# Optimization experiments

Hardware: AMD Instinct MI355X
Metric: run time of the kernel (lower is better)

Reference implementation:

```python
import jax, jax.numpy as jnp
import numpy as np

NUM_HEAD = 16


def setup_inputs() -> dict:
    key = jax.random.key(0)
    ks = jax.random.split(key, 4)
    B, C, D = 2, 2048, 1024
    hidden_states = jax.random.normal(ks[0], (B, C, D), dtype=jnp.float32)
    attention_mask = jnp.zeros((B, 1, C, C), dtype=jnp.float32)
    Wqkv = jax.random.normal(ks[1], (D, 3 * D), dtype=jnp.float32) * (D ** -0.5)
    bqkv = jnp.zeros((3 * D,), dtype=jnp.float32)
    Wo = jax.random.normal(ks[2], (D, D), dtype=jnp.float32) * (D ** -0.5)
    bo = jnp.zeros((D,), dtype=jnp.float32)
    return {"hidden_states": hidden_states, "attention_mask": attention_mask,
            "Wqkv": Wqkv, "bqkv": bqkv, "Wo": Wo, "bo": bo}


def reference(hidden_states, attention_mask, Wqkv, bqkv, Wo, bo):
    B, C, D = hidden_states.shape
    H = NUM_HEAD
    hd = D // H
    scaling = hd ** -0.5

    qkv = hidden_states @ Wqkv + bqkv                      # [B, C, 3D]
    q, k, v = jnp.split(qkv, 3, axis=-1)
    # [B, C, H, hd] -> [B, H, C, hd]
    q = q.reshape(B, C, H, hd).transpose(0, 2, 1, 3)
    k = k.reshape(B, C, H, hd).transpose(0, 2, 1, 3)
    v = v.reshape(B, C, H, hd).transpose(0, 2, 1, 3)

    scores = jnp.einsum("bhqd,bhkd->bhqk", q, k) * scaling  # [B, H, C, C]
    causal = jnp.tril(jnp.ones((C, C), dtype=bool))[None, None]
    mask = jnp.where(causal, attention_mask, -jnp.inf)      # [B, 1, C, C]
    probs = jax.nn.softmax(scores + mask, axis=-1)
    out = jnp.einsum("bhqk,bhkd->bhqd", probs, v)           # [B, H, C, hd]
    out = out.transpose(0, 2, 1, 3).reshape(B, C, D)
    return out @ Wo + bo
```

## Files before the change

### kernel.cpp

```cpp
#include <hip/hip_runtime.h>
#include <hip/hip_bf16.h>
#include <cstdint>
#include <cstddef>

typedef __attribute__((ext_vector_type(8))) short short8;
typedef __attribute__((ext_vector_type(4))) float f32x4;
typedef __attribute__((ext_vector_type(16))) float f32x16;
typedef __attribute__((ext_vector_type(4))) unsigned int u32x4;
typedef unsigned short u16;
typedef unsigned int u32;

#define B_ 2
#define C_ 2048
#define D_ 1024
#define H_ 16
#define HD_ 64
#define LOG2E 1.4426950408889634f

static __device__ __forceinline__ u16 f2b(float f) {
  u32 x = __builtin_bit_cast(u32, f);
  x += 0x7FFFu + ((x >> 16) & 1u);
  return (u16)(x >> 16);
}
static __device__ __forceinline__ float b2f(u16 v) {
  return __builtin_bit_cast(float, (u32)v << 16);
}

__device__ const unsigned char SEGTAB[20] = {
  1, 66, 67, 83, 132, 148, 133, 149, 165, 198, 214, 230, 199, 215, 231, 247,
  0, 82, 164, 246};

__global__ void k_convert(const float* __restrict__ in, u16* __restrict__ out, int n) {
  int i = (blockIdx.x * blockDim.x + threadIdx.x) * 4;
  const int stride = gridDim.x * blockDim.x * 4;
  for (; i < n; i += stride) {
    float4 v = *reinterpret_cast<const float4*>(in + i);
    ushort4 o;
    o.x = f2b(v.x); o.y = f2b(v.y); o.z = f2b(v.z); o.w = f2b(v.w);
    *reinterpret_cast<ushort4*>(out + i) = o;
  }
}

__global__ void k_tconv(const float* __restrict__ in, u16* __restrict__ out, int R, int Cc) {
  __shared__ float tile[64][65];
  const int tC = blockIdx.x * 64;
  const int tR = blockIdx.y * 64;
  const int t = threadIdx.x;
  const int r0 = t >> 4;
  const int c0 = (t & 15) * 4;
#pragma unroll
  for (int ii = 0; ii < 4; ++ii) {
    int r = ii * 16 + r0;
    float4 v = *reinterpret_cast<const float4*>(&in[(size_t)(tR + r) * Cc + tC + c0]);
    tile[r][c0] = v.x; tile[r][c0 + 1] = v.y; tile[r][c0 + 2] = v.z; tile[r][c0 + 3] = v.w;
  }
  __syncthreads();
#pragma unroll
  for (int ii = 0; ii < 4; ++ii) {
    int c = ii * 16 + r0;
    ushort4 o;
    o.x = f2b(tile[c0 + 0][c]);
    o.y = f2b(tile[c0 + 1][c]);
    o.z = f2b(tile[c0 + 2][c]);
    o.w = f2b(tile[c0 + 3][c]);
    *reinterpret_cast<ushort4*>(&out[(size_t)(tC + c) * R + tR + c0]) = o;
  }
}

__global__ void k_maskflags(const float* __restrict__ mask, u32* __restrict__ flags) {
  const int bid = blockIdx.x;
  const int kt = bid & 31, qs = (bid >> 5) & 31, b = bid >> 10;
  const int t = threadIdx.x;
  const float* base = mask + ((size_t)b * C_ + qs * 64) * C_ + kt * 64;
  const int row = t >> 2, c0 = (t & 3) * 16;
  int any = 0;
#pragma unroll
  for (int i = 0; i < 4; ++i) {
    float4 v = *reinterpret_cast<const float4*>(base + (size_t)row * C_ + c0 + i * 4);
    any |= (v.x != 0.f) | (v.y != 0.f) | (v.z != 0.f) | (v.w != 0.f);
  }
  __shared__ int sh[4];
  const unsigned long long bal = __ballot(any);
  if ((t & 63) == 0) sh[t >> 6] = (bal != 0ull);
  __syncthreads();
  if (t == 0) flags[bid] = (u32)(sh[0] | sh[1] | sh[2] | sh[3]);
}

#define GLL16(gptr, lptr) __builtin_amdgcn_global_load_lds( \
    (const __attribute__((address_space(1))) u32*)(gptr),   \
    (__attribute__((address_space(3))) u32*)(lptr), 16, 0, 0)

template<int EPI, int BM>
__global__ __launch_bounds__(256) void k_gemm(
    const u16* __restrict__ A, const u16* __restrict__ Bt,
    int M, int N, int K, const float* __restrict__ bias,
    u16* __restrict__ Cq, u16* __restrict__ Ck, u16* __restrict__ Cv,
    float* __restrict__ Cf)
{
  constexpr int WCW = (BM == 128) ? 64 : 32;
  constexpr int NF = WCW / 16;
  __shared__ __align__(16) u16 As[BM * 64];
  __shared__ __align__(16) u16 Bs[128 * 64];
  const int t = threadIdx.x;
  const int l = t & 63, w = t >> 6;
  const int wr = (BM == 128) ? (w >> 1) : 0;
  const int wc = (BM == 128) ? (w & 1) : w;
  const int lr = l & 15, lg = l >> 4;
  const int swk = lr & 7;
  const int m0 = blockIdx.y * BM, n0 = blockIdx.x * 128;
  f32x4 acc[4][NF] = {};

  for (int k0 = 0; k0 < K; k0 += 64) {
#pragma unroll
    for (int s = 0; s < BM / 32; ++s) {
      const int u = s * 256 + t;
      const int row = u >> 3, slot = (u & 7) ^ (row & 7);
      GLL16(A + (size_t)(m0 + row) * K + k0 + (slot << 3), As + (u << 3));
    }
#pragma unroll
    for (int s = 0; s < 4; ++s) {
      const int u = s * 256 + t;
      const int row = u >> 3, slot = (u & 7) ^ (row & 7);
      GLL16(Bt + (size_t)(n0 + row) * K + k0 + (slot << 3), Bs + (u << 3));
    }
    __syncthreads();
    short8 af[2][4], bfr[2][NF];
#pragma unroll
    for (int s = 0; s < 2; ++s) {
#pragma unroll
      for (int m = 0; m < 4; ++m)
        af[s][m] = *reinterpret_cast<const short8*>(
            &As[((wr * 64 + m * 16 + lr) << 6) + (((s * 4 + lg) ^ swk) << 3)]);
#pragma unroll
      for (int n = 0; n < NF; ++n)
        bfr[s][n] = *reinterpret_cast<const short8*>(
            &Bs[((wc * WCW + n * 16 + lr) << 6) + (((s * 4 + lg) ^ swk) << 3)]);
    }
#pragma unroll
    for (int s = 0; s < 2; ++s)
#pragma unroll
      for (int m = 0; m < 4; ++m)
#pragma unroll
        for (int n = 0; n < NF; ++n)
          acc[m][n] = __builtin_amdgcn_mfma_f32_16x16x32_bf16(af[s][m], bfr[s][n], acc[m][n], 0, 0, 0);
    __syncthreads();
  }

#pragma unroll
  for (int m = 0; m < 4; ++m) {
    const int mg = m0 + wr * 64 + m * 16 + lg * 4;
    const int bq = mg >> 11, c0 = mg & 2047;
#pragma unroll
    for (int n = 0; n < NF; ++n) {
      const int ng = n0 + wc * WCW + n * 16 + lr;
      const float bia = bias[ng];
      if (EPI == 0) {
        const int reg = ng >> 10, d = ng & 1023, h = d >> 6, e = d & 63;
        if (reg == 2) {
          u16* vp = Cv + (((size_t)(bq * H_ + h) * HD_ + e) << 11) + c0;
#pragma unroll
          for (int j = 0; j < 4; ++j) vp[j] = f2b(acc[m][n][j] + bia);
        } else {
          u16* dst = (reg == 0) ? Cq : Ck;
#pragma unroll
          for (int j = 0; j < 4; ++j)
            dst[(((size_t)(bq * H_ + h) * C_ + c0 + j) << 6) + e] = f2b(acc[m][n][j] + bia);
        }
      } else {
#pragma unroll
        for (int j = 0; j < 4; ++j)
          Cf[(size_t)(mg + j) * N + ng] = acc[m][n][j] + bia;
      }
    }
  }
}

static __device__ __forceinline__ void stage_kv(
    const u16* __restrict__ Kbh, const u16* __restrict__ Vbh,
    u16* Kd, u16* Vd, int kt, int t)
{
  const int row = t >> 3, slot = (t & 7) ^ (row & 7);
  GLL16(Kbh + (((size_t)(kt * 64 + row)) << 6) + (slot << 3), Kd + (t << 3));
  GLL16(Vbh + (((size_t)row) << 11) + kt * 64 + (slot << 3), Vd + (t << 3));
}

__global__ __launch_bounds__(512) void k_attn(
    const u16* __restrict__ Q, const u16* __restrict__ Kb, const u16* __restrict__ Vt,
    const float* __restrict__ mask, const u32* __restrict__ flags,
    u16* __restrict__ O, u16* __restrict__ Opart, float2* __restrict__ ml)
{
  __shared__ __align__(16) u16 buf[3 * 8192];
  const int bid = blockIdx.x;
  const int bh = bid & 31;
  const int e = SEGTAB[bid >> 5];
  const int qt = e & 15, seg = (e >> 4) & 3, nseg = (e >> 6) + 1;
  const int ntiles = 4 * qt + 4;
  const int kt0 = seg * 8;
  const int kt1 = (kt0 + 8 < ntiles) ? kt0 + 8 : ntiles;
  const int slotbase = (qt < 4) ? (qt - 2) * 2
                     : (qt < 6) ? 4 + (qt - 4) * 3
                     : 10 + (qt - 6) * 4;
  const int slot = bh * 18 + slotbase + seg;

  const int b = bh >> 4, h = bh & 15;
  const int t = threadIdx.x;
  const int l = t & 63, w = t >> 6;
  const int q = l & 31, hi = l >> 5;
  const int q7 = q & 7;

  const u16* Kbh = Kb + (size_t)bh * (C_ * HD_);
  const u16* Vbh = Vt + (size_t)bh * (HD_ * C_);

  const int q0w = qt * 256 + w * 32;
  const int qg = q0w + q;
  const int qmaxw = q0w + 31;

  short8 aq[4];
  {
    const u16* qp = Q + ((size_t)bh * C_ + qg) * HD_ + hi * 8;
#pragma unroll
    for (int kh = 0; kh < 4; ++kh) {
      short8 v = *reinterpret_cast<const short8*>(qp + kh * 16);
#pragma unroll
      for (int i = 0; i < 8; ++i) {
        const float f = b2f((u16)v[i]) * (0.125f * LOG2E);
        v[i] = (short)f2b(f);
      }
      aq[kh] = v;
    }
  }

  u32 fbits = 0;
  {
    const u32* fp = flags + (size_t)(b * 32 + (q0w >> 6)) * 32 + kt0;
#pragma unroll
    for (int i = 0; i < 8; ++i) fbits |= (fp[i] ? 1u : 0u) << i;
  }

  f32x16 oa0 = {}, oa1 = {};
  float mrun = -INFINITY, srun = 0.f;
  const float* mrow = mask + ((size_t)b * C_ + qg) * C_;

  stage_kv(Kbh, Vbh, buf, buf + 4096, kt0, t);
  if (kt0 + 1 < kt1) stage_kv(Kbh, Vbh, buf + 8192, buf + 8192 + 4096, kt0 + 1, t);

#pragma unroll 1
  for (int kt = kt0; kt < kt1; ++kt) {
    const int bi = (kt - kt0) % 3;
    if (kt + 1 < kt1) asm volatile("s_waitcnt vmcnt(2)" ::: "memory");
    else              asm volatile("s_waitcnt vmcnt(0)" ::: "memory");
    __builtin_amdgcn_s_barrier();
    __builtin_amdgcn_sched_barrier(0);
    if (kt + 2 < kt1) {
      const int bn = (kt + 2 - kt0) % 3;
      stage_kv(Kbh, Vbh, buf + bn * 8192, buf + bn * 8192 + 4096, kt + 2, t);
    }
    if (kt * 64 > qmaxw) continue;

    const char* Kc = reinterpret_cast<const char*>(buf + bi * 8192);
    const char* Vc = reinterpret_cast<const char*>(buf + bi * 8192 + 4096);

    f32x16 p0 = {}, p1 = {};
#pragma unroll
    for (int kh = 0; kh < 4; ++kh) {
      const int sl = ((2 * kh + hi) ^ q7) << 4;
      const short8 k0 = *reinterpret_cast<const short8*>(Kc + q * 128 + sl);
      const short8 k1 = *reinterpret_cast<const short8*>(Kc + (32 + q) * 128 + sl);
      p0 = __builtin_amdgcn_mfma_f32_32x32x16_bf16(k0, aq[kh], p0, 0, 0, 0);
      p1 = __builtin_amdgcn_mfma_f32_32x32x16_bf16(k1, aq[kh], p1, 0, 0, 0);
    }

    if ((fbits >> (kt - kt0)) & 1u) {
      const float* mp = mrow + kt * 64 + 4 * hi;
#pragma unroll
      for (int g = 0; g < 4; ++g) {
        const float4 m0 = *reinterpret_cast<const float4*>(mp + 8 * g);
        const float4 m1 = *reinterpret_cast<const float4*>(mp + 32 + 8 * g);
        p0[4*g+0] = fmaf(m0.x, LOG2E, p0[4*g+0]);
        p0[4*g+1] = fmaf(m0.y, LOG2E, p0[4*g+1]);
        p0[4*g+2] = fmaf(m0.z, LOG2E, p0[4*g+2]);
        p0[4*g+3] = fmaf(m0.w, LOG2E, p0[4*g+3]);
        p1[4*g+0] = fmaf(m1.x, LOG2E, p1[4*g+0]);
        p1[4*g+1] = fmaf(m1.y, LOG2E, p1[4*g+1]);
        p1[4*g+2] = fmaf(m1.z, LOG2E, p1[4*g+2]);
        p1[4*g+3] = fmaf(m1.w, LOG2E, p1[4*g+3]);
      }
    }
    if (kt * 64 + 63 > q0w) {
#pragma unroll
      for (int r = 0; r < 16; ++r) {
        const int kl = kt * 64 + (r & 3) + 8 * (r >> 2) + 4 * hi;
        if (kl > qg) p0[r] = -INFINITY;
        if (kl + 32 > qg) p1[r] = -INFINITY;
      }
    }

    float pm = -INFINITY;
#pragma unroll
    for (int r = 0; r < 16; ++r) pm = fmaxf(pm, fmaxf(p0[r], p1[r]));
    pm = fmaxf(pm, __shfl_xor(pm, 32));
    if (__ballot(pm > mrun) != 0ull) {
      const float mn = fmaxf(fmaxf(mrun, pm), -1e30f);
      const float rs = exp2f(mrun - mn);
      srun *= rs;
      oa0 *= rs; oa1 *= rs;
      mrun = mn;
    }
    float sum = 0.f;
#pragma unroll
    for (int r = 0; r < 16; ++r) {
      p0[r] = exp2f(p0[r] - mrun); sum += p0[r];
      p1[r] = exp2f(p1[r] - mrun); sum += p1[r];
    }
    sum += __shfl_xor(sum, 32);
    srun += sum;

    __builtin_amdgcn_s_setprio(1);
#pragma unroll
    for (int ks = 0; ks < 4; ++ks) {
      const int o = (ks & 1) * 8;
      u32 X, X2, Y, Y2;
      if (ks < 2) {
        asm("v_cvt_pk_bf16_f32 %0, %1, %2" : "=v"(X)  : "v"(p0[o+0]), "v"(p0[o+1]));
        asm("v_cvt_pk_bf16_f32 %0, %1, %2" : "=v"(X2) : "v"(p0[o+2]), "v"(p0[o+3]));
        asm("v_cvt_pk_bf16_f32 %0, %1, %2" : "=v"(Y)  : "v"(p0[o+4]), "v"(p0[o+5]));
        asm("v_cvt_pk_bf16_f32 %0, %1, %2" : "=v"(Y2) : "v"(p0[o+6]), "v"(p0[o+7]));
      } else {
        asm("v_cvt_pk_bf16_f32 %0, %1, %2" : "=v"(X)  : "v"(p1[o+0]), "v"(p1[o+1]));
        asm("v_cvt_pk_bf16_f32 %0, %1, %2" : "=v"(X2) : "v"(p1[o+2]), "v"(p1[o+3]));
        asm("v_cvt_pk_bf16_f32 %0, %1, %2" : "=v"(Y)  : "v"(p1[o+4]), "v"(p1[o+5]));
        asm("v_cvt_pk_bf16_f32 %0, %1, %2" : "=v"(Y2) : "v"(p1[o+6]), "v"(p1[o+7]));
      }
      asm("v_permlane32_swap_b32 %0, %1" : "+v"(X), "+v"(Y));
      asm("v_permlane32_swap_b32 %0, %1" : "+v"(X2), "+v"(Y2));
      const u32x4 bw = {X, X2, Y, Y2};
      const short8 bp = __builtin_bit_cast(short8, bw);
      const int sl = ((2 * ks + hi) ^ q7) << 4;
      const short8 v0 = *reinterpret_cast<const short8*>(Vc + q * 128 + sl);
      const short8 v1 = *reinterpret_cast<const short8*>(Vc + (32 + q) * 128 + sl);
      oa0 = __builtin_amdgcn_mfma_f32_32x32x16_bf16(v0, bp, oa0, 0, 0, 0);
      oa1 = __builtin_amdgcn_mfma_f32_32x32x16_bf16(v1, bp, oa1, 0, 0, 0);
    }
    __builtin_amdgcn_s_setprio(0);
  }

  const float rinv = 1.f / srun;
  const int q2 = l >> 1, hf = l & 1;
#pragma unroll 1
  for (int ph = 0; ph < 2; ++ph) {
    __syncthreads();
    if ((w >> 2) == ph) {
      char* Swb = reinterpret_cast<char*>(buf) + (w & 3) * 4608;
#pragma unroll
      for (int g = 0; g < 4; ++g) {
        const int d0 = 8 * g + 4 * hi;
        const float a0 = oa0[4*g+0] * rinv, a1 = oa0[4*g+1] * rinv;
        const float a2 = oa0[4*g+2] * rinv, a3 = oa0[4*g+3] * rinv;
        const float b0 = oa1[4*g+0] * rinv, b1 = oa1[4*g+1] * rinv;
        const float b2 = oa1[4*g+2] * rinv, b3 = oa1[4*g+3] * rinv;
        u32 w0, w1, w2, w3;
        asm("v_cvt_pk_bf16_f32 %0, %1, %2" : "=v"(w0) : "v"(a0), "v"(a1));
        asm("v_cvt_pk_bf16_f32 %0, %1, %2" : "=v"(w1) : "v"(a2), "v"(a3));
        asm("v_cvt_pk_bf16_f32 %0, %1, %2" : "=v"(w2) : "v"(b0), "v"(b1));
        asm("v_cvt_pk_bf16_f32 %0, %1, %2" : "=v"(w3) : "v"(b2), "v"(b3));
        *reinterpret_cast<uint2*>(Swb + q * 144 + d0 * 2) = make_uint2(w0, w1);
        *reinterpret_cast<uint2*>(Swb + q * 144 + (d0 + 32) * 2) = make_uint2(w2, w3);
      }
      asm volatile("" ::: "memory");
      if (nseg == 1) {
        u16* orow = O + ((size_t)b * C_ + q0w + q2) * D_ + h * 64 + hf * 32;
#pragma unroll
        for (int i = 0; i < 4; ++i) {
          const short8 v = *reinterpret_cast<const short8*>(Swb + q2 * 144 + hf * 64 + i * 16);
          *reinterpret_cast<short8*>(orow + i * 8) = v;
        }
      } else {
        u16* prow = Opart + (((size_t)slot * 256 + w * 32 + q2) << 6) + hf * 32;
#pragma unroll
        for (int i = 0; i < 4; ++i) {
          const short8 v = *reinterpret_cast<const short8*>(Swb + q2 * 144 + hf * 64 + i * 16);
          *reinterpret_cast<short8*>(prow + i * 8) = v;
        }
      }
    }
  }
  if (nseg > 1 && hi == 0)
    ml[(size_t)slot * 256 + w * 32 + q] = make_float2(mrun, srun);
}

__global__ __launch_bounds__(512) void k_merge(
    const u16* __restrict__ Opart, const float2* __restrict__ ml, u16* __restrict__ O)
{
  const int bid = blockIdx.x;
  const int bh = bid & 31;
  const int qt = 2 + (bid >> 5);
  const int nseg = (qt < 4) ? 2 : (qt < 6) ? 3 : 4;
  const int slotbase = (qt < 4) ? (qt - 2) * 2
                     : (qt < 6) ? 4 + (qt - 4) * 3
                     : 10 + (qt - 6) * 4;
  const int slot0 = bh * 18 + slotbase;
  const int b = bh >> 4, h = bh & 15;
  const int t = threadIdx.x;
  const int q = t >> 1, dh = t & 1;

  float m[4], l_[4];
  float M = -INFINITY;
#pragma unroll 4
  for (int s = 0; s < nseg; ++s) {
    const float2 v = ml[(size_t)(slot0 + s) * 256 + q];
    m[s] = v.x; l_[s] = v.y;
    M = fmaxf(M, v.x);
  }
  float a[4], L = 0.f;
#pragma unroll 4
  for (int s = 0; s < nseg; ++s) { a[s] = exp2f(m[s] - M) * l_[s]; L += a[s]; }
  const float rL = 1.f / L;

  float acc[32] = {};
#pragma unroll 4
  for (int s = 0; s < nseg; ++s) {
    const u16* op = Opart + (((size_t)(slot0 + s) * 256 + q) << 6) + dh * 32;
    const float ws = a[s] * rL;
#pragma unroll
    for (int i = 0; i < 4; ++i) {
      const short8 v = *reinterpret_cast<const short8*>(op + i * 8);
#pragma unroll
      for (int j = 0; j < 8; ++j) acc[i * 8 + j] += ws * b2f((u16)v[j]);
    }
  }
  u16* orow = O + ((size_t)b * C_ + qt * 256 + q) * D_ + h * 64 + dh * 32;
#pragma unroll
  for (int i = 0; i < 4; ++i) {
    short8 v;
#pragma unroll
    for (int j = 0; j < 8; ++j) v[j] = (short)f2b(acc[i * 8 + j]);
    *reinterpret_cast<short8*>(orow + i * 8) = v;
  }
}

extern "C" void kernel_launch(void* const* d_in, const int* in_sizes, int n_in,
                              void* d_out, int out_size, void* d_ws, size_t ws_size,
                              hipStream_t stream) {
  const float* hs   = (const float*)d_in[0];
  const float* mask = (const float*)d_in[1];
  const float* Wqkv = (const float*)d_in[2];
  const float* bqkv = (const float*)d_in[3];
  const float* Wo   = (const float*)d_in[4];
  const float* bo   = (const float*)d_in[5];
  float* out = (float*)d_out;
  char* ws = (char*)d_ws;

  u16*    hsb   = (u16*)(ws);
  u16*    Opart = (u16*)(ws);
  u16*    Wqkvt = (u16*)(ws + (8  << 20));
  float2* mlbuf = (float2*)(ws + (19 << 20));
  u32*    flags = (u32*)(ws + (20 << 20) + (1 << 19));
  u16*    Wot   = (u16*)(ws + (21 << 20));
  u16*    Qb    = (u16*)(ws + (24 << 20));
  u16*    Kb    = (u16*)(ws + (32 << 20));
  u16*    Vtb   = (u16*)(ws + (40 << 20));
  u16*    AOb   = (u16*)(ws + (48 << 20));

  k_convert<<<2048, 256, 0, stream>>>(hs, hsb, 4096 * 1024);
  k_tconv<<<dim3(3072 / 64, 1024 / 64), 256, 0, stream>>>(Wqkv, Wqkvt, 1024, 3072);
  k_tconv<<<dim3(1024 / 64, 1024 / 64), 256, 0, stream>>>(Wo, Wot, 1024, 1024);
  k_maskflags<<<2048, 256, 0, stream>>>(mask, flags);
  k_gemm<0, 128><<<dim3(24, 32), 256, 0, stream>>>(hsb, Wqkvt, 4096, 3072, 1024, bqkv,
                                                   Qb, Kb, Vtb, nullptr);
  k_attn<<<640, 512, 0, stream>>>(Qb, Kb, Vtb, mask, flags, AOb, Opart, mlbuf);
  k_merge<<<192, 512, 0, stream>>>(Opart, mlbuf, AOb);
  k_gemm<1, 64><<<dim3(8, 64), 256, 0, stream>>>(AOb, Wot, 4096, 1024, 1024, bo,
                                                 nullptr, nullptr, nullptr, out);
}
```

Measured before the change: 136.7 us.

## Fuse prep kernels, load K/V directly to registers, add lazy softmax rescale

Merges the four preprocessing launches (activation convert, two weight transposes, mask flag scan) into one multi-role kernel to cut launch overhead. The attention kernel drops its shared-memory triple-buffered K/V staging and block barriers. Each wave now loads its own K and V fragments from global memory into registers and stops at its own causal bound. It also rescales the running max only when it grows by more than 8 in log2 units, and the epilogue uses per-wave shared scratch with no block sync. The risks are more global/L2 traffic from redundant per-wave K/V loads and possible exposed memory latency without the software pipeline.

Result: slower. 153.0 us (+11.9%).

```diff
diff --git a/kernel.cpp b/kernel.cpp
--- a/kernel.cpp
+++ b/kernel.cpp
@@ -30,22 +30,10 @@
   1, 66, 67, 83, 132, 148, 133, 149, 165, 198, 214, 230, 199, 215, 231, 247,
   0, 82, 164, 246};
 
-__global__ void k_convert(const float* __restrict__ in, u16* __restrict__ out, int n) {
-  int i = (blockIdx.x * blockDim.x + threadIdx.x) * 4;
-  const int stride = gridDim.x * blockDim.x * 4;
-  for (; i < n; i += stride) {
-    float4 v = *reinterpret_cast<const float4*>(in + i);
-    ushort4 o;
-    o.x = f2b(v.x); o.y = f2b(v.y); o.z = f2b(v.z); o.w = f2b(v.w);
-    *reinterpret_cast<ushort4*>(out + i) = o;
-  }
-}
-
-__global__ void k_tconv(const float* __restrict__ in, u16* __restrict__ out, int R, int Cc) {
-  __shared__ float tile[64][65];
-  const int tC = blockIdx.x * 64;
-  const int tR = blockIdx.y * 64;
-  const int t = threadIdx.x;
+static __device__ void tconv_body(const float* __restrict__ in, u16* __restrict__ out,
+                                  int R, int Cc, int bx, int by, int t,
+                                  float (*tile)[65]) {
+  const int tC = bx * 64, tR = by * 64;
   const int r0 = t >> 4;
   const int c0 = (t & 15) * 4;
 #pragma unroll
@@ -67,23 +55,48 @@
   }
 }
 
-__global__ void k_maskflags(const float* __restrict__ mask, u32* __restrict__ flags) {
+__global__ __launch_bounds__(256) void k_prep(
+    const float* __restrict__ hs, u16* __restrict__ hsb,
+    const float* __restrict__ Wqkv, u16* __restrict__ Wqkvt,
+    const float* __restrict__ Wo, u16* __restrict__ Wot,
+    const float* __restrict__ mask, u32* __restrict__ flags)
+{
+  __shared__ float tile[64][65];
+  __shared__ int sh[4];
   const int bid = blockIdx.x;
-  const int kt = bid & 31, qs = (bid >> 5) & 31, b = bid >> 10;
   const int t = threadIdx.x;
-  const float* base = mask + ((size_t)b * C_ + qs * 64) * C_ + kt * 64;
-  const int row = t >> 2, c0 = (t & 3) * 16;
-  int any = 0;
-#pragma unroll
-  for (int i = 0; i < 4; ++i) {
-    float4 v = *reinterpret_cast<const float4*>(base + (size_t)row * C_ + c0 + i * 4);
-    any |= (v.x != 0.f) | (v.y != 0.f) | (v.z != 0.f) | (v.w != 0.f);
-  }
-  __shared__ int sh[4];
-  const unsigned long long bal = __ballot(any);
-  if ((t & 63) == 0) sh[t >> 6] = (bal != 0ull);
-  __syncthreads();
-  if (t == 0) flags[bid] = (u32)(sh[0] | sh[1] | sh[2] | sh[3]);
+  if (bid < 2048) {
+    int i = (bid * 256 + t) * 4;
+    const int n = 4096 * 1024;
+    const int stride = 2048 * 256 * 4;
+    for (; i < n; i += stride) {
+      float4 v = *reinterpret_cast<const float4*>(hs + i);
+      ushort4 o;
+      o.x = f2b(v.x); o.y = f2b(v.y); o.z = f2b(v.z); o.w = f2b(v.w);
+      *reinterpret_cast<ushort4*>(hsb + i) = o;
+    }
+  } else if (bid < 2816) {
+    const int r = bid - 2048;
+    tconv_body(Wqkv, Wqkvt, 1024, 3072, r % 48, r / 48, t, tile);
+  } else if (bid < 3072) {
+    const int r = bid - 2816;
+    tconv_body(Wo, Wot, 1024, 1024, r % 16, r / 16, t, tile);
+  } else {
+    const int mb = bid - 3072;
+    const int kt = mb & 31, qs = (mb >> 5) & 31, b = mb >> 10;
+    const float* base = mask + ((size_t)b * C_ + qs * 64) * C_ + kt * 64;
+    const int row = t >> 2, c0 = (t & 3) * 16;
+    int any = 0;
+#pragma unroll
+    for (int i = 0; i < 4; ++i) {
+      float4 v = *reinterpret_cast<const float4*>(base + (size_t)row * C_ + c0 + i * 4);
+      any |= (v.x != 0.f) | (v.y != 0.f) | (v.z != 0.f) | (v.w != 0.f);
+    }
+    const unsigned long long bal = __ballot(any);
+    if ((t & 63) == 0) sh[t >> 6] = (bal != 0ull);
+    __syncthreads();
+    if (t == 0) flags[mb] = (u32)(sh[0] | sh[1] | sh[2] | sh[3]);
+  }
 }
 
 #define GLL16(gptr, lptr) __builtin_amdgcn_global_load_lds( \
@@ -175,21 +188,12 @@
   }
 }
 
-static __device__ __forceinline__ void stage_kv(
-    const u16* __restrict__ Kbh, const u16* __restrict__ Vbh,
-    u16* Kd, u16* Vd, int kt, int t)
-{
-  const int row = t >> 3, slot = (t & 7) ^ (row & 7);
-  GLL16(Kbh + (((size_t)(kt * 64 + row)) << 6) + (slot << 3), Kd + (t << 3));
-  GLL16(Vbh + (((size_t)row) << 11) + kt * 64 + (slot << 3), Vd + (t << 3));
-}
-
 __global__ __launch_bounds__(512) void k_attn(
     const u16* __restrict__ Q, const u16* __restrict__ Kb, const u16* __restrict__ Vt,
     const float* __restrict__ mask, const u32* __restrict__ flags,
     u16* __restrict__ O, u16* __restrict__ Opart, float2* __restrict__ ml)
 {
-  __shared__ __align__(16) u16 buf[3 * 8192];
+  __shared__ __align__(16) u16 sep[8][2304];
   const int bid = blockIdx.x;
   const int bh = bid & 31;
   const int e = SEGTAB[bid >> 5];
@@ -206,7 +210,6 @@
   const int t = threadIdx.x;
   const int l = t & 63, w = t >> 6;
   const int q = l & 31, hi = l >> 5;
-  const int q7 = q & 7;
 
   const u16* Kbh = Kb + (size_t)bh * (C_ * HD_);
   const u16* Vbh = Vt + (size_t)bh * (HD_ * C_);
@@ -214,6 +217,7 @@
   const int q0w = qt * 256 + w * 32;
   const int qg = q0w + q;
   const int qmaxw = q0w + 31;
+  const int ktw1 = min(kt1, (qmaxw >> 6) + 1);
 
   short8 aq[4];
   {
@@ -241,33 +245,32 @@
   float mrun = -INFINITY, srun = 0.f;
   const float* mrow = mask + ((size_t)b * C_ + qg) * C_;
 
-  stage_kv(Kbh, Vbh, buf, buf + 4096, kt0, t);
-  if (kt0 + 1 < kt1) stage_kv(Kbh, Vbh, buf + 8192, buf + 8192 + 4096, kt0 + 1, t);
+  const u16* kb0 = Kbh + (((size_t)q) << 6) + hi * 8;
+  const u16* vb0 = Vbh + (((size_t)q) << 11) + hi * 8;
 
 #pragma unroll 1
-  for (int kt = kt0; kt < kt1; ++kt) {
-    const int bi = (kt - kt0) % 3;
-    if (kt + 1 < kt1) asm volatile("s_waitcnt vmcnt(2)" ::: "memory");
-    else              asm volatile("s_waitcnt vmcnt(0)" ::: "memory");
-    __builtin_amdgcn_s_barrier();
-    __builtin_amdgcn_sched_barrier(0);
-    if (kt + 2 < kt1) {
-      const int bn = (kt + 2 - kt0) % 3;
-      stage_kv(Kbh, Vbh, buf + bn * 8192, buf + bn * 8192 + 4096, kt + 2, t);
-    }
-    if (kt * 64 > qmaxw) continue;
-
-    const char* Kc = reinterpret_cast<const char*>(buf + bi * 8192);
-    const char* Vc = reinterpret_cast<const char*>(buf + bi * 8192 + 4096);
-
+  for (int kt = kt0; kt < ktw1; ++kt) {
+    const u16* kp0 = kb0 + ((size_t)kt << 12);
+    const u16* kp1 = kp0 + (32 << 6);
+    short8 k0r[4], k1r[4];
+#pragma unroll
+    for (int kh = 0; kh < 4; ++kh) {
+      k0r[kh] = *reinterpret_cast<const short8*>(kp0 + kh * 16);
+      k1r[kh] = *reinterpret_cast<const short8*>(kp1 + kh * 16);
+    }
     f32x16 p0 = {}, p1 = {};
 #pragma unroll
     for (int kh = 0; kh < 4; ++kh) {
-      const int sl = ((2 * kh + hi) ^ q7) << 4;
-      const short8 k0 = *reinterpret_cast<const short8*>(Kc + q * 128 + sl);
-      const short8 k1 = *reinterpret_cast<const short8*>(Kc + (32 + q) * 128 + sl);
-      p0 = __builtin_amdgcn_mfma_f32_32x32x16_bf16(k0, aq[kh], p0, 0, 0, 0);
-      p1 = __builtin_amdgcn_mfma_f32_32x32x16_bf16(k1, aq[kh], p1, 0, 0, 0);
+      p0 = __builtin_amdgcn_mfma_f32_32x32x16_bf16(k0r[kh], aq[kh], p0, 0, 0, 0);
+      p1 = __builtin_amdgcn_mfma_f32_32x32x16_bf16(k1r[kh], aq[kh], p1, 0, 0, 0);
+    }
+    const u16* vp0 = vb0 + kt * 64;
+    const u16* vp1 = vp0 + (32 << 11);
+    short8 v0r[4], v1r[4];
+#pragma unroll
+    for (int ks = 0; ks < 4; ++ks) {
+      v0r[ks] = *reinterpret_cast<const short8*>(vp0 + ks * 16);
+      v1r[ks] = *reinterpret_cast<const short8*>(vp1 + ks * 16);
     }
 
     if ((fbits >> (kt - kt0)) & 1u) {
@@ -299,7 +302,7 @@
 #pragma unroll
     for (int r = 0; r < 16; ++r) pm = fmaxf(pm, fmaxf(p0[r], p1[r]));
     pm = fmaxf(pm, __shfl_xor(pm, 32));
-    if (__ballot(pm > mrun) != 0ull) {
+    if (__ballot(pm > mrun + 8.f) != 0ull) {
       const float mn = fmaxf(fmaxf(mrun, pm), -1e30f);
       const float rs = exp2f(mrun - mn);
       srun *= rs;
@@ -335,57 +338,47 @@
       asm("v_permlane32_swap_b32 %0, %1" : "+v"(X2), "+v"(Y2));
       const u32x4 bw = {X, X2, Y, Y2};
       const short8 bp = __builtin_bit_cast(short8, bw);
-      const int sl = ((2 * ks + hi) ^ q7) << 4;
-      const short8 v0 = *reinterpret_cast<const short8*>(Vc + q * 128 + sl);
-      const short8 v1 = *reinterpret_cast<const short8*>(Vc + (32 + q) * 128 + sl);
-      oa0 = __builtin_amdgcn_mfma_f32_32x32x16_bf16(v0, bp, oa0, 0, 0, 0);
-      oa1 = __builtin_amdgcn_mfma_f32_32x32x16_bf16(v1, bp, oa1, 0, 0, 0);
+      oa0 = __builtin_amdgcn_mfma_f32_32x32x16_bf16(v0r[ks], bp, oa0, 0, 0, 0);
+      oa1 = __builtin_amdgcn_mfma_f32_32x32x16_bf16(v1r[ks], bp, oa1, 0, 0, 0);
     }
     __builtin_amdgcn_s_setprio(0);
   }
 
   const float rinv = 1.f / srun;
+  char* Swb = reinterpret_cast<char*>(sep[w]);
+#pragma unroll
+  for (int g = 0; g < 4; ++g) {
+    const int d0 = 8 * g + 4 * hi;
+    const float a0 = oa0[4*g+0] * rinv, a1 = oa0[4*g+1] * rinv;
+    const float a2 = oa0[4*g+2] * rinv, a3 = oa0[4*g+3] * rinv;
+    const float b0 = oa1[4*g+0] * rinv, b1 = oa1[4*g+1] * rinv;
+    const float b2 = oa1[4*g+2] * rinv, b3 = oa1[4*g+3] * rinv;
+    u32 w0, w1, w2, w3;
+    asm("v_cvt_pk_bf16_f32 %0, %1, %2" : "=v"(w0) : "v"(a0), "v"(a1));
+    asm("v_cvt_pk_bf16_f32 %0, %1, %2" : "=v"(w1) : "v"(a2), "v"(a3));
+    asm("v_cvt_pk_bf16_f32 %0, %1, %2" : "=v"(w2) : "v"(b0), "v"(b1));
+    asm("v_cvt_pk_bf16_f32 %0, %1, %2" : "=v"(w3) : "v"(b2), "v"(b3));
+    *reinterpret_cast<uint2*>(Swb + q * 144 + d0 * 2) = make_uint2(w0, w1);
+    *reinterpret_cast<uint2*>(Swb + q * 144 + (d0 + 32) * 2) = make_uint2(w2, w3);
+  }
+  asm volatile("" ::: "memory");
   const int q2 = l >> 1, hf = l & 1;
-#pragma unroll 1
-  for (int ph = 0; ph < 2; ++ph) {
-    __syncthreads();
-    if ((w >> 2) == ph) {
-      char* Swb = reinterpret_cast<char*>(buf) + (w & 3) * 4608;
-#pragma unroll
-      for (int g = 0; g < 4; ++g) {
-        const int d0 = 8 * g + 4 * hi;
-        const float a0 = oa0[4*g+0] * rinv, a1 = oa0[4*g+1] * rinv;
-        const float a2 = oa0[4*g+2] * rinv, a3 = oa0[4*g+3] * rinv;
-        const float b0 = oa1[4*g+0] * rinv, b1 = oa1[4*g+1] * rinv;
-        const float b2 = oa1[4*g+2] * rinv, b3 = oa1[4*g+3] * rinv;
-        u32 w0, w1, w2, w3;
-        asm("v_cvt_pk_bf16_f32 %0, %1, %2" : "=v"(w0) : "v"(a0), "v"(a1));
-        asm("v_cvt_pk_bf16_f32 %0, %1, %2" : "=v"(w1) : "v"(a2), "v"(a3));
-        asm("v_cvt_pk_bf16_f32 %0, %1, %2" : "=v"(w2) : "v"(b0), "v"(b1));
-        asm("v_cvt_pk_bf16_f32 %0, %1, %2" : "=v"(w3) : "v"(b2), "v"(b3));
-        *reinterpret_cast<uint2*>(Swb + q * 144 + d0 * 2) = make_uint2(w0, w1);
-        *reinterpret_cast<uint2*>(Swb + q * 144 + (d0 + 32) * 2) = make_uint2(w2, w3);
-      }
-      asm volatile("" ::: "memory");
-      if (nseg == 1) {
-        u16* orow = O + ((size_t)b * C_ + q0w + q2) * D_ + h * 64 + hf * 32;
-#pragma unroll
-        for (int i = 0; i < 4; ++i) {
-          const short8 v = *reinterpret_cast<const short8*>(Swb + q2 * 144 + hf * 64 + i * 16);
-          *reinterpret_cast<short8*>(orow + i * 8) = v;
-        }
-      } else {
-        u16* prow = Opart + (((size_t)slot * 256 + w * 32 + q2) << 6) + hf * 32;
-#pragma unroll
-        for (int i = 0; i < 4; ++i) {
-          const short8 v = *reinterpret_cast<const short8*>(Swb + q2 * 144 + hf * 64 + i * 16);
-          *reinterpret_cast<short8*>(prow + i * 8) = v;
-        }
-      }
-    }
-  }
-  if (nseg > 1 && hi == 0)
-    ml[(size_t)slot * 256 + w * 32 + q] = make_float2(mrun, srun);
+  if (nseg == 1) {
+    u16* orow = O + ((size_t)b * C_ + q0w + q2) * D_ + h * 64 + hf * 32;
+#pragma unroll
+    for (int i = 0; i < 4; ++i) {
+      const short8 v = *reinterpret_cast<const short8*>(Swb + q2 * 144 + hf * 64 + i * 16);
+      *reinterpret_cast<short8*>(orow + i * 8) = v;
+    }
+  } else {
+    u16* prow = Opart + (((size_t)slot * 256 + w * 32 + q2) << 6) + hf * 32;
+#pragma unroll
+    for (int i = 0; i < 4; ++i) {
+      const short8 v = *reinterpret_cast<const short8*>(Swb + q2 * 144 + hf * 64 + i * 16);
+      *reinterpret_cast<short8*>(prow + i * 8) = v;
+    }
+    if (hi == 0) ml[(size_t)slot * 256 + w * 32 + q] = make_float2(mrun, srun);
+  }
 }
 
 __global__ __launch_bounds__(512) void k_merge(
@@ -461,10 +454,7 @@
   u16*    Vtb   = (u16*)(ws + (40 << 20));
   u16*    AOb   = (u16*)(ws + (48 << 20));
 
-  k_convert<<<2048, 256, 0, stream>>>(hs, hsb, 4096 * 1024);
-  k_tconv<<<dim3(3072 / 64, 1024 / 64), 256, 0, stream>>>(Wqkv, Wqkvt, 1024, 3072);
-  k_tconv<<<dim3(1024 / 64, 1024 / 64), 256, 0, stream>>>(Wo, Wot, 1024, 1024);
-  k_maskflags<<<2048, 256, 0, stream>>>(mask, flags);
+  k_prep<<<5120, 256, 0, stream>>>(hs, hsb, Wqkv, Wqkvt, Wo, Wot, mask, flags);
   k_gemm<0, 128><<<dim3(24, 32), 256, 0, stream>>>(hsb, Wqkvt, 4096, 3072, 1024, bqkv,
                                                    Qb, Kb, Vtb, nullptr);
   k_attn<<<640, 512, 0, stream>>>(Qb, Kb, Vtb, mask, flags, AOb, Opart, mlbuf);
```
